# Performance work log

Measured on AMD Instinct MI355X. Metric: run time of the kernel, lower is better.

## Reference

```python
import jax, jax.numpy as jnp
import numpy as np
from jax import lax

B, C, H, W = 2, 64, 128, 128
F_SCALE, STRIDE = 2, 2
F = F_SCALE * STRIDE            # pixel-unshuffle factor = 4
CK = C // 16                    # attention channel dim = 4
SCALE_DIM = C // F_SCALE        # softmax scale uses embed_size//f_scale = 32


def setup_inputs() -> dict:
    key = jax.random.key(0)
    ks = jax.random.split(key, 16)
    g = lambda i, shape, s=0.05: jax.random.normal(ks[i], shape, jnp.float32) * s
    return {
        "x":   jax.random.normal(ks[0], (B, C, H, W), jnp.float32),
        # conv1 = Sequential(1x1 C->CK, 1x1 CK->CK)
        "w1a": g(1, (CK, C)), "b1a": g(2, (CK,)),
        "w1b": g(3, (CK, CK)), "b1b": g(4, (CK,)),
        # wqk parameter (torch.randn, std 1)
        "wqk": jax.random.normal(ks[5], (CK, CK), jnp.float32),
        # conv2: 1x1 CK->C ; conv: 1x1 C->C
        "w2":  g(6, (C, CK)), "b2": g(7, (C,)),
        "wc":  g(8, (C, C)), "bc": g(9, (C,)),
        # FF (GridSANaive): 1x1 C->C/4, 3x3 dilated C/4->C/4, 1x1 C/4->C
        "wf1": g(10, (C // 4, C)), "bf1": g(11, (C // 4,)),
        "wf2": g(12, (C // 4, C // 4, 3, 3)), "bf2": g(13, (C // 4,)),
        "wf3": g(14, (C, C // 4)), "bf3": g(15, (C,)),
    }


def conv1x1(x, w, b):
    return jnp.einsum('bchw,oc->bohw', x, w) + b[None, :, None, None]


def grid_attention(x, wqk):
    b, c, h, w = x.shape
    sh = h // 2
    x = jnp.pad(x, ((0, 0), (0, 0), (sh, 0), (0, 0)))      # Shift2d pad (top)
    # F.layer_norm over last 3 dims, no affine, eps=1e-5
    mu = jnp.mean(x, axis=(1, 2, 3), keepdims=True)
    var = jnp.var(x, axis=(1, 2, 3), keepdims=True)
    xx = (x - mu) / jnp.sqrt(var + 1e-5)
    hh, ww = xx.shape[2], xx.shape[3]
    ph, pw = (F - hh % F) % F, (F - ww % F) % F
    xx = jnp.pad(xx, ((0, 0), (0, 0), (0, ph), (0, pw)))
    gh, gw = (hh + ph) // F, (ww + pw) // F
    # pixel_unshuffle: channel layout (c, fy, fx)
    xx = xx.reshape(b, c, gh, F, gw, F).transpose(0, 1, 3, 5, 2, 4)
    xx = xx.reshape(b, c * F * F, gh, gw)
    # rearrange 'b (f c) h w -> (b f) c h w', f=F*F (mixes layout, as in original)
    xx = xx.reshape(b * F * F, c, gh, gw)
    L = gh * gw
    tok = xx.transpose(0, 2, 3, 1).reshape(b * F * F, L, c)   # (bg, L, c)
    qk = tok @ wqk
    qk = qk / (jnp.linalg.norm(qk, axis=-1, keepdims=True) + 1e-8)
    attn = (jnp.einsum('blk,bmk->blm', qk, qk) + 1.0) / (SCALE_DIM ** 0.5)
    attn = jax.nn.softmax(attn, axis=-1)
    out = jnp.einsum('blm,bmc->blc', attn, tok)
    out = out.reshape(b * F * F, gh, gw, c).transpose(0, 3, 1, 2)
    out = out.reshape(b, F * F * c, gh, gw)
    # pixel_shuffle: channel layout (fy, fx, c)
    out = out.reshape(b, F, F, c, gh, gw).transpose(0, 3, 4, 1, 5, 2)
    out = out.reshape(b, c, gh * F, gw * F)
    out = out[:, :, :hh, :ww]                               # undo shuffle pad
    return out[:, :, :-sh, :] if sh > 0 else out            # Shift2d crop (bottom)


def ff(x, wf1, bf1, wf2, bf2, wf3, bf3):
    h1 = jax.nn.relu(conv1x1(x, wf1, bf1))
    k = 1 + (STRIDE // 2) * 2   # ShiftConv2d offset for 3x3, dilation=STRIDE
    hp = jnp.pad(h1, ((0, 0), (0, 0), (k, 0), (0, 0)))
    h2 = lax.conv_general_dilated(
        hp, wf2, (1, 1), ((STRIDE, STRIDE), (STRIDE, STRIDE)),
        rhs_dilation=(STRIDE, STRIDE),
        dimension_numbers=('NCHW', 'OIHW', 'NCHW'))
    h2 = jax.nn.relu((h2 + bf2[None, :, None, None])[:, :, :-k, :])
    return conv1x1(h2, wf3, bf3)


def reference(x, w1a, b1a, w1b, b1b, wqk, w2, b2, wc, bc,
              wf1, bf1, wf2, bf2, wf3, bf3):
    a = conv1x1(conv1x1(x, w1a, b1a), w1b, b1b)
    att = grid_attention(a, wqk)
    y = x + conv1x1(conv1x1(att, w2, b2), wc, bc)
    return y + ff(y, wf1, bf1, wf2, bf2, wf3, bf3)
```

## Files before the change

kernel.cpp:

```cpp
#include <hip/hip_runtime.h>
#include <math.h>

#define CHW  (64*16384)
#define ATT_SCALE 0.17677669529663687f

__device__ __forceinline__ float poly_exp(float d) {
  return 1.f + d*(1.f + d*(0.5f + d*(0.16666667f + d*0.04166667f)));
}

__global__ __launch_bounds__(256) void k1_a_stats(
    const float* __restrict__ x, const float* __restrict__ w1a,
    const float* __restrict__ b1a, const float* __restrict__ w1b,
    const float* __restrict__ b1b, float* __restrict__ a,
    float* __restrict__ statsbuf) {
  __shared__ float sA[256];
  __shared__ float sb1[4];
  __shared__ float pc[4][4][256];
  __shared__ float rs[64], rq[64];
  int tid = threadIdx.x;
  {
    int o = tid >> 6, c = tid & 63;
    float s = 0.f;
    #pragma unroll
    for (int k = 0; k < 4; ++k) s += w1b[o*4+k] * w1a[k*64+c];
    sA[tid] = s;
  }
  if (tid < 4) {
    float s = b1b[tid];
    #pragma unroll
    for (int k = 0; k < 4; ++k) s += w1b[tid*4+k] * b1a[k];
    sb1[tid] = s;
  }
  __syncthreads();
  int quad = tid & 15, cg = tid >> 4;
  int gq = blockIdx.x * 16 + quad;
  int bb = gq >> 12;
  int px0 = (gq & 4095) * 4;
  const float* xp = x + bb*CHW + (cg*4)*16384 + px0;
  float4 acc[4];
  #pragma unroll
  for (int o = 0; o < 4; ++o) acc[o] = make_float4(0.f,0.f,0.f,0.f);
  #pragma unroll
  for (int cc = 0; cc < 4; ++cc) {
    float4 xv = *(const float4*)(xp + cc*16384);
    int c = cg*4 + cc;
    #pragma unroll
    for (int o = 0; o < 4; ++o) {
      float w = sA[o*64+c];
      acc[o].x += w*xv.x; acc[o].y += w*xv.y; acc[o].z += w*xv.z; acc[o].w += w*xv.w;
    }
  }
  #pragma unroll
  for (int o = 0; o < 4; ++o) {
    pc[0][o][tid] = acc[o].x; pc[1][o][tid] = acc[o].y;
    pc[2][o][tid] = acc[o].z; pc[3][o][tid] = acc[o].w;
  }
  __syncthreads();
  if (tid < 64) {
    int q2 = tid & 15, o = tid >> 4;
    float sx=0.f, sy=0.f, sz=0.f, sw=0.f;
    #pragma unroll
    for (int g2 = 0; g2 < 16; ++g2) {
      int idx = g2*16 + q2;
      sx += pc[0][o][idx]; sy += pc[1][o][idx];
      sz += pc[2][o][idx]; sw += pc[3][o][idx];
    }
    float bv = sb1[o];
    sx += bv; sy += bv; sz += bv; sw += bv;
    int gq2 = blockIdx.x*16 + q2;
    int b2 = gq2 >> 12; int p0 = (gq2 & 4095)*4;
    *(float4*)(a + b2*4*16384 + o*16384 + p0) = make_float4(sx,sy,sz,sw);
    rs[tid] = sx+sy+sz+sw;
    rq[tid] = sx*sx+sy*sy+sz*sz+sw*sw;
  }
  __syncthreads();
  for (int s2 = 32; s2; s2 >>= 1) {
    if (tid < s2) { rs[tid] += rs[tid+s2]; rq[tid] += rq[tid+s2]; }
    __syncthreads();
  }
  if (tid == 0) { statsbuf[blockIdx.x*2] = rs[0]; statsbuf[blockIdx.x*2+1] = rq[0]; }
}

__global__ __launch_bounds__(512) void k23_attn(
    const float* __restrict__ a, const float* __restrict__ statsbuf,
    const float* __restrict__ wqk, float* __restrict__ att) {
  __shared__ float4 kq[1024];
  __shared__ float4 kt[1024];
  __shared__ float red[8][5][64];
  __shared__ float padr[8][5];
  __shared__ float swqk[16];
  __shared__ float padout[4];
  __shared__ float smu[2];
  int tid = threadIdx.x;
  if (tid < 64) {
    float s1 = 0.f, s2 = 0.f;
    #pragma unroll
    for (int r = 0; r < 8; ++r) {
      s1 += statsbuf[2*(tid*8+r)];
      s2 += statsbuf[2*(tid*8+r)+1];
    }
    #pragma unroll
    for (int m = 1; m < 64; m <<= 1) {
      s1 += __shfl_xor(s1, m);
      s2 += __shfl_xor(s2, m);
    }
    if (tid == 0) { smu[0] = s1; smu[1] = s2; }
  }
  if (tid < 16) swqk[tid] = wqk[tid];
  __syncthreads();
  float mu  = smu[0] * (1.f/98304.f);
  float var = smu[1] * (1.f/98304.f) - mu*mu;
  float rsig = rsqrtf(var + 1e-5f);
  int g = blockIdx.x >> 3, qb = blockIdx.x & 7;
  int b = g >> 4, u = (g >> 2) & 3, v = g & 3;
  const float* abase = a + ((b*4+u) << 14);
  for (int km = tid; km < 1024; km += 512) {
    int tt = 512 + km;
    int i = tt >> 5, j = tt & 31;
    int row = (i - 16)*4 + v;
    float4 tv = *(const float4*)(abase + row*128 + (j << 2));
    tv.x = (tv.x-mu)*rsig; tv.y = (tv.y-mu)*rsig;
    tv.z = (tv.z-mu)*rsig; tv.w = (tv.w-mu)*rsig;
    float q0 = tv.x*swqk[0] + tv.y*swqk[4] + tv.z*swqk[8]  + tv.w*swqk[12];
    float q1 = tv.x*swqk[1] + tv.y*swqk[5] + tv.z*swqk[9]  + tv.w*swqk[13];
    float q2 = tv.x*swqk[2] + tv.y*swqk[6] + tv.z*swqk[10] + tv.w*swqk[14];
    float q3 = tv.x*swqk[3] + tv.y*swqk[7] + tv.z*swqk[11] + tv.w*swqk[15];
    float nrm = sqrtf(q0*q0 + q1*q1 + q2*q2 + q3*q3);
    float inv = 1.f / (nrm + 1e-8f);
    kt[km] = tv;
    kq[km] = make_float4(q0*inv, q1*inv, q2*inv, q3*inv);
  }
  float tpad = -mu * rsig;
  float c0 = swqk[0]+swqk[4]+swqk[8]+swqk[12];
  float c1 = swqk[1]+swqk[5]+swqk[9]+swqk[13];
  float c2 = swqk[2]+swqk[6]+swqk[10]+swqk[14];
  float c3 = swqk[3]+swqk[7]+swqk[11]+swqk[15];
  float p0 = tpad*c0, p1 = tpad*c1, p2 = tpad*c2, p3 = tpad*c3;
  float pn = sqrtf(p0*p0+p1*p1+p2*p2+p3*p3);
  float pinv = 1.f / (pn + 1e-8f);
  float4 qpu = make_float4(p0*pinv, p1*pinv, p2*pinv, p3*pinv);
  __syncthreads();
  int s = tid >> 5, qi = tid & 31;
  float4 q[2];
  #pragma unroll
  for (int j = 0; j < 2; ++j) {
    float4 vq = kq[qb*64 + j*32 + qi];
    q[j] = make_float4(vq.x*ATT_SCALE, vq.y*ATT_SCALE, vq.z*ATT_SCALE, vq.w*ATT_SCALE);
  }
  float den[2] = {0.f, 0.f};
  float4 ov[2];
  ov[0] = make_float4(0.f,0.f,0.f,0.f); ov[1] = make_float4(0.f,0.f,0.f,0.f);
  if (s == 0) {
    #pragma unroll
    for (int j = 0; j < 2; ++j) {
      float d = q[j].x*qpu.x + q[j].y*qpu.y + q[j].z*qpu.z + q[j].w*qpu.w;
      float e = 512.f * poly_exp(d);
      den[j] += e;
      ov[j].x += e*tpad; ov[j].y += e*tpad; ov[j].z += e*tpad; ov[j].w += e*tpad;
    }
  }
  int m0 = s * 64;
  #pragma unroll 2
  for (int m = m0; m < m0 + 64; ++m) {
    float4 kk = kq[m];
    float4 tv = kt[m];
    #pragma unroll
    for (int j = 0; j < 2; ++j) {
      float d = q[j].x*kk.x + q[j].y*kk.y + q[j].z*kk.z + q[j].w*kk.w;
      float e = poly_exp(d);
      den[j] += e;
      ov[j].x += e*tv.x; ov[j].y += e*tv.y; ov[j].z += e*tv.z; ov[j].w += e*tv.w;
    }
  }
  #pragma unroll
  for (int j = 0; j < 2; ++j) {
    den[j]  += __shfl_xor(den[j], 32);
    ov[j].x += __shfl_xor(ov[j].x, 32);
    ov[j].y += __shfl_xor(ov[j].y, 32);
    ov[j].z += __shfl_xor(ov[j].z, 32);
    ov[j].w += __shfl_xor(ov[j].w, 32);
  }
  if ((tid & 32) == 0) {
    int hs = s >> 1;
    #pragma unroll
    for (int j = 0; j < 2; ++j) {
      int slot = j*32 + qi;
      red[hs][0][slot] = den[j];
      red[hs][1][slot] = ov[j].x; red[hs][2][slot] = ov[j].y;
      red[hs][3][slot] = ov[j].z; red[hs][4][slot] = ov[j].w;
    }
  }
  {
    float4 qs = make_float4(qpu.x*ATT_SCALE, qpu.y*ATT_SCALE, qpu.z*ATT_SCALE, qpu.w*ATT_SCALE);
    float pd = 0.f, px = 0.f, py = 0.f, pz = 0.f, pw = 0.f;
    #pragma unroll
    for (int mm = 0; mm < 2; ++mm) {
      int m = tid + mm*512;
      float4 kk = kq[m]; float4 tv = kt[m];
      float d = qs.x*kk.x + qs.y*kk.y + qs.z*kk.z + qs.w*kk.w;
      float e = poly_exp(d);
      pd += e; px += e*tv.x; py += e*tv.y; pz += e*tv.z; pw += e*tv.w;
    }
    if (tid == 0) {
      float d = qs.x*qpu.x + qs.y*qpu.y + qs.z*qpu.z + qs.w*qpu.w;
      float e = 512.f * poly_exp(d);
      pd += e; px += e*tpad; py += e*tpad; pz += e*tpad; pw += e*tpad;
    }
    #pragma unroll
    for (int mask = 1; mask < 64; mask <<= 1) {
      pd += __shfl_xor(pd, mask);
      px += __shfl_xor(px, mask); py += __shfl_xor(py, mask);
      pz += __shfl_xor(pz, mask); pw += __shfl_xor(pw, mask);
    }
    if ((tid & 63) == 0) {
      int wv = tid >> 6;
      padr[wv][0] = pd; padr[wv][1] = px; padr[wv][2] = py;
      padr[wv][3] = pz; padr[wv][4] = pw;
    }
  }
  __syncthreads();
  if (tid < 64) {
    float dsum=0.f, ox=0.f, oy=0.f, oz=0.f, ow=0.f;
    #pragma unroll
    for (int ss = 0; ss < 8; ++ss) {
      dsum += red[ss][0][tid];
      ox += red[ss][1][tid]; oy += red[ss][2][tid];
      oz += red[ss][3][tid]; ow += red[ss][4][tid];
    }
    float inv = 1.f / dsum;
    int t = 512 + qb*64 + tid;
    int i = t >> 5, j = t & 31;
    float* ap = att + b*65536 + (i*4+u)*128 + (j*4+v);
    ap[0]     = ox*inv;
    ap[16384] = oy*inv;
    ap[32768] = oz*inv;
    ap[49152] = ow*inv;
  } else if (tid == 64) {
    float dsum=0.f, ox=0.f, oy=0.f, oz=0.f, ow=0.f;
    #pragma unroll
    for (int wv = 0; wv < 8; ++wv) {
      dsum += padr[wv][0];
      ox += padr[wv][1]; oy += padr[wv][2]; oz += padr[wv][3]; ow += padr[wv][4];
    }
    float inv = 1.f / dsum;
    padout[0] = ox*inv; padout[1] = oy*inv; padout[2] = oz*inv; padout[3] = ow*inv;
  }
  __syncthreads();
  if (qb == 0) {
    int i = tid >> 5, j = tid & 31;
    float* ap = att + b*65536 + (i*4+u)*128 + (j*4+v);
    ap[0] = padout[0]; ap[16384] = padout[1];
    ap[32768] = padout[2]; ap[49152] = padout[3];
  }
}

__global__ __launch_bounds__(256) void k4_y_h1(
    const float* __restrict__ x, const float* __restrict__ att,
    const float* __restrict__ w2p, const float* __restrict__ b2p,
    const float* __restrict__ wcp, const float* __restrict__ bcp,
    const float* __restrict__ wf1, const float* __restrict__ bf1,
    float* __restrict__ yout, float* __restrict__ h1) {
  __shared__ float4 sWf4[64];
  __shared__ float sbfc[64];
  __shared__ float sw1t[1024];
  __shared__ float sb1[16];
  __shared__ float4 satt[4][8];
  __shared__ float4 ylds[64][8];
  int tid = threadIdx.x;
  {
    int o = tid >> 2, k = tid & 3;
    float s = 0.f;
    for (int c = 0; c < 64; ++c) s += wcp[o*64+c] * w2p[c*4+k];
    ((float*)&sWf4[o])[k] = s;
  }
  if (tid < 64) {
    float s = bcp[tid];
    for (int c = 0; c < 64; ++c) s += wcp[tid*64+c] * b2p[c];
    sbfc[tid] = s;
  }
  for (int i = tid; i < 1024; i += 256) {
    int c = i >> 4, o2 = i & 15;
    sw1t[i] = wf1[o2*64 + c];
  }
  if (tid < 16) sb1[tid] = bf1[tid];
  int quad = tid & 7, og = tid >> 3;
  int gq = blockIdx.x*8 + quad;
  int bb = gq >> 12, px0 = (gq & 4095)*4;
  if (tid < 32) {
    int k = tid >> 3, q2 = tid & 7;
    int gq2 = blockIdx.x*8 + q2;
    int b2i = gq2 >> 12, p0 = (gq2 & 4095)*4;
    satt[k][q2] = *(const float4*)(att + b2i*65536 + k*16384 + p0);
  }
  __syncthreads();
  float4 a0 = satt[0][quad], a1 = satt[1][quad], a2 = satt[2][quad], a3 = satt[3][quad];
  const float* xp = x + bb*CHW + px0;
  float* yp = yout + bb*CHW + px0;
  #pragma unroll
  for (int cc = 0; cc < 2; ++cc) {
    int c = og*2 + cc;
    float4 xv = *(const float4*)(xp + c*16384);
    float4 wf = sWf4[c];
    float bv = sbfc[c];
    float4 yv;
    yv.x = xv.x + wf.x*a0.x + wf.y*a1.x + wf.z*a2.x + wf.w*a3.x + bv;
    yv.y = xv.y + wf.x*a0.y + wf.y*a1.y + wf.z*a2.y + wf.w*a3.y + bv;
    yv.z = xv.z + wf.x*a0.z + wf.y*a1.z + wf.z*a2.z + wf.w*a3.z + bv;
    yv.w = xv.w + wf.x*a0.w + wf.y*a1.w + wf.z*a2.w + wf.w*a3.w + bv;
    *(float4*)(yp + c*16384) = yv;
    ylds[c][quad] = yv;
  }
  __syncthreads();
  if (og < 16) {
    float bv = sb1[og];
    float4 acc = make_float4(bv, bv, bv, bv);
    #pragma unroll 8
    for (int c = 0; c < 64; ++c) {
      float w = sw1t[c*16 + og];
      float4 yv = ylds[c][quad];
      acc.x += w*yv.x; acc.y += w*yv.y; acc.z += w*yv.z; acc.w += w*yv.w;
    }
    acc.x = fmaxf(acc.x,0.f); acc.y = fmaxf(acc.y,0.f);
    acc.z = fmaxf(acc.z,0.f); acc.w = fmaxf(acc.w,0.f);
    *(float4*)(h1 + bb*262144 + og*16384 + px0) = acc;
  }
}

__global__ __launch_bounds__(256) void k6_ff_out(
    const float* __restrict__ h1, const float* __restrict__ wf2,
    const float* __restrict__ bf2, const float* __restrict__ wf3,
    const float* __restrict__ bf3, float* yo) {
  __shared__ float sbuf[16][3][40];
  __shared__ float sW2t[2304];
  __shared__ float sw3[1024];
  __shared__ float sb2[16], sb3[64];
  __shared__ float sh2[32][17];
  int tid = threadIdx.x;
  int bi = blockIdx.x;
  int bb = bi >> 9, h = (bi >> 2) & 127, wq = bi & 3;
  int W0 = wq * 32;
  for (int idx = tid; idx < 1920; idx += 256) {
    int c = idx / 120;
    int rem = idx % 120;
    int r = rem / 40, cl = rem % 40;
    int row = h - 5 + 2*r;
    int gw = W0 - 4 + cl;
    float v = 0.f;
    if (row >= 0 && gw >= 0 && gw < 128)
      v = h1[bb*262144 + c*16384 + row*128 + gw];
    sbuf[c][r][cl] = v;
  }
  for (int i2 = tid; i2 < 2304; i2 += 256) {
    int o2 = i2 & 15, rest = i2 >> 4;
    int t = rest % 3, r = (rest/3) % 3, c = rest/9;
    sW2t[i2] = wf2[((o2*16 + c)*3 + r)*3 + t];
  }
  for (int i2 = tid; i2 < 1024; i2 += 256) sw3[i2] = wf3[i2];
  if (tid < 16) sb2[tid] = bf2[tid];
  else if (tid < 80) sb3[tid-16] = bf3[tid-16];
  __syncthreads();
  int w = tid & 31, og = tid >> 5;
  float acc0 = sb2[og*2], acc1 = sb2[og*2+1];
  #pragma unroll 4
  for (int c = 0; c < 16; ++c) {
    #pragma unroll
    for (int r = 0; r < 3; ++r) {
      float tm = sbuf[c][r][w+2];
      float t0 = sbuf[c][r][w+4];
      float tp = sbuf[c][r][w+6];
      int base = ((c*3 + r)*3) << 4;
      acc0 += sW2t[base + og*2]      * tm + sW2t[base + 16 + og*2]     * t0 + sW2t[base + 32 + og*2]     * tp;
      acc1 += sW2t[base + og*2 + 1]  * tm + sW2t[base + 16 + og*2 + 1] * t0 + sW2t[base + 32 + og*2 + 1] * tp;
    }
  }
  sh2[w][og*2]   = fmaxf(acc0, 0.f);
  sh2[w][og*2+1] = fmaxf(acc1, 0.f);
  __syncthreads();
  float hv[16];
  #pragma unroll
  for (int k = 0; k < 16; ++k) hv[k] = sh2[w][k];
  float* ybase = yo + bb*CHW + h*128 + W0 + w;
  #pragma unroll 2
  for (int oc = 0; oc < 8; ++oc) {
    int o = og*8 + oc;
    float sv = sb3[o] + ybase[o*16384];
    const float* s3 = &sw3[o*16];
    #pragma unroll
    for (int k = 0; k < 16; ++k) sv += s3[k]*hv[k];
    ybase[o*16384] = sv;
  }
}

extern "C" void kernel_launch(void* const* d_in, const int* in_sizes, int n_in,
                              void* d_out, int out_size, void* d_ws, size_t ws_size,
                              hipStream_t stream) {
  (void)in_sizes; (void)n_in; (void)out_size; (void)ws_size;
  const float* x   = (const float*)d_in[0];
  const float* w1a = (const float*)d_in[1];
  const float* b1a = (const float*)d_in[2];
  const float* w1b = (const float*)d_in[3];
  const float* b1b = (const float*)d_in[4];
  const float* wqk = (const float*)d_in[5];
  const float* w2  = (const float*)d_in[6];
  const float* b2  = (const float*)d_in[7];
  const float* wc  = (const float*)d_in[8];
  const float* bc  = (const float*)d_in[9];
  const float* wf1 = (const float*)d_in[10];
  const float* bf1 = (const float*)d_in[11];
  const float* wf2 = (const float*)d_in[12];
  const float* bf2 = (const float*)d_in[13];
  const float* wf3 = (const float*)d_in[14];
  const float* bf3 = (const float*)d_in[15];

  float* ws = (float*)d_ws;
  float* a_    = ws;
  float* stats = ws + 131072;
  float* att   = ws + 132096;
  float* h1    = ws + 263168;
  float* y     = (float*)d_out;

  k1_a_stats<<<512,  256, 0, stream>>>(x, w1a, b1a, w1b, b1b, a_, stats);
  k23_attn  <<<256,  512, 0, stream>>>(a_, stats, wqk, att);
  k4_y_h1   <<<1024, 256, 0, stream>>>(x, att, w2, b2, wc, bc, wf1, bf1, y, h1);
  k6_ff_out <<<1024, 256, 0, stream>>>(h1, wf2, bf2, wf3, bf3, y);
}
```

Before: 138.4 us.

## Fuse four kernels into one cooperative persistent kernel with grid syncs

Replaces the four separate launches with a single cooperative kernel of 256 blocks of 512 threads that runs each stage in turn, separated by grid-wide syncs. Shared memory is one raw buffer reused by every stage, and each stage's work per block is remapped: stage 1 handles 32 quads per block, and the FF stage handles a full image row per block. The folded conv2/conv weights are computed once by block 0 and written to the workspace instead of being recomputed by every block. This removes inter-kernel launch gaps, but only 256 blocks cover the whole GPU, so the bandwidth-heavy stages may lose parallelism and occupancy.

Measured after the change: 231.1 us. 67.0% more time.

```diff
diff --git a/kernel.cpp b/kernel.cpp
--- a/kernel.cpp
+++ b/kernel.cpp
@@ -1,5 +1,8 @@
 #include <hip/hip_runtime.h>
+#include <hip/hip_cooperative_groups.h>
 #include <math.h>
+
+namespace cg = cooperative_groups;
 
 #define CHW  (64*16384)
 #define ATT_SCALE 0.17677669529663687f
@@ -8,386 +11,407 @@
   return 1.f + d*(1.f + d*(0.5f + d*(0.16666667f + d*0.04166667f)));
 }
 
-__global__ __launch_bounds__(256) void k1_a_stats(
+__global__ __launch_bounds__(512) void mega(
     const float* __restrict__ x, const float* __restrict__ w1a,
     const float* __restrict__ b1a, const float* __restrict__ w1b,
-    const float* __restrict__ b1b, float* __restrict__ a,
-    float* __restrict__ statsbuf) {
-  __shared__ float sA[256];
-  __shared__ float sb1[4];
-  __shared__ float pc[4][4][256];
-  __shared__ float rs[64], rq[64];
-  int tid = threadIdx.x;
-  {
-    int o = tid >> 6, c = tid & 63;
-    float s = 0.f;
-    #pragma unroll
-    for (int k = 0; k < 4; ++k) s += w1b[o*4+k] * w1a[k*64+c];
-    sA[tid] = s;
-  }
-  if (tid < 4) {
-    float s = b1b[tid];
-    #pragma unroll
-    for (int k = 0; k < 4; ++k) s += w1b[tid*4+k] * b1a[k];
-    sb1[tid] = s;
-  }
-  __syncthreads();
-  int quad = tid & 15, cg = tid >> 4;
-  int gq = blockIdx.x * 16 + quad;
-  int bb = gq >> 12;
-  int px0 = (gq & 4095) * 4;
-  const float* xp = x + bb*CHW + (cg*4)*16384 + px0;
-  float4 acc[4];
-  #pragma unroll
-  for (int o = 0; o < 4; ++o) acc[o] = make_float4(0.f,0.f,0.f,0.f);
-  #pragma unroll
-  for (int cc = 0; cc < 4; ++cc) {
-    float4 xv = *(const float4*)(xp + cc*16384);
-    int c = cg*4 + cc;
-    #pragma unroll
-    for (int o = 0; o < 4; ++o) {
-      float w = sA[o*64+c];
-      acc[o].x += w*xv.x; acc[o].y += w*xv.y; acc[o].z += w*xv.z; acc[o].w += w*xv.w;
-    }
-  }
-  #pragma unroll
-  for (int o = 0; o < 4; ++o) {
-    pc[0][o][tid] = acc[o].x; pc[1][o][tid] = acc[o].y;
-    pc[2][o][tid] = acc[o].z; pc[3][o][tid] = acc[o].w;
-  }
-  __syncthreads();
-  if (tid < 64) {
-    int q2 = tid & 15, o = tid >> 4;
-    float sx=0.f, sy=0.f, sz=0.f, sw=0.f;
-    #pragma unroll
-    for (int g2 = 0; g2 < 16; ++g2) {
-      int idx = g2*16 + q2;
-      sx += pc[0][o][idx]; sy += pc[1][o][idx];
-      sz += pc[2][o][idx]; sw += pc[3][o][idx];
-    }
-    float bv = sb1[o];
-    sx += bv; sy += bv; sz += bv; sw += bv;
-    int gq2 = blockIdx.x*16 + q2;
-    int b2 = gq2 >> 12; int p0 = (gq2 & 4095)*4;
-    *(float4*)(a + b2*4*16384 + o*16384 + p0) = make_float4(sx,sy,sz,sw);
-    rs[tid] = sx+sy+sz+sw;
-    rq[tid] = sx*sx+sy*sy+sz*sz+sw*sw;
-  }
-  __syncthreads();
-  for (int s2 = 32; s2; s2 >>= 1) {
-    if (tid < s2) { rs[tid] += rs[tid+s2]; rq[tid] += rq[tid+s2]; }
-    __syncthreads();
-  }
-  if (tid == 0) { statsbuf[blockIdx.x*2] = rs[0]; statsbuf[blockIdx.x*2+1] = rq[0]; }
-}
-
-__global__ __launch_bounds__(512) void k23_attn(
-    const float* __restrict__ a, const float* __restrict__ statsbuf,
-    const float* __restrict__ wqk, float* __restrict__ att) {
-  __shared__ float4 kq[1024];
-  __shared__ float4 kt[1024];
-  __shared__ float red[8][5][64];
-  __shared__ float padr[8][5];
-  __shared__ float swqk[16];
-  __shared__ float padout[4];
-  __shared__ float smu[2];
-  int tid = threadIdx.x;
-  if (tid < 64) {
-    float s1 = 0.f, s2 = 0.f;
-    #pragma unroll
-    for (int r = 0; r < 8; ++r) {
-      s1 += statsbuf[2*(tid*8+r)];
-      s2 += statsbuf[2*(tid*8+r)+1];
-    }
-    #pragma unroll
-    for (int m = 1; m < 64; m <<= 1) {
-      s1 += __shfl_xor(s1, m);
-      s2 += __shfl_xor(s2, m);
-    }
-    if (tid == 0) { smu[0] = s1; smu[1] = s2; }
-  }
-  if (tid < 16) swqk[tid] = wqk[tid];
-  __syncthreads();
-  float mu  = smu[0] * (1.f/98304.f);
-  float var = smu[1] * (1.f/98304.f) - mu*mu;
-  float rsig = rsqrtf(var + 1e-5f);
-  int g = blockIdx.x >> 3, qb = blockIdx.x & 7;
-  int b = g >> 4, u = (g >> 2) & 3, v = g & 3;
-  const float* abase = a + ((b*4+u) << 14);
-  for (int km = tid; km < 1024; km += 512) {
-    int tt = 512 + km;
-    int i = tt >> 5, j = tt & 31;
-    int row = (i - 16)*4 + v;
-    float4 tv = *(const float4*)(abase + row*128 + (j << 2));
-    tv.x = (tv.x-mu)*rsig; tv.y = (tv.y-mu)*rsig;
-    tv.z = (tv.z-mu)*rsig; tv.w = (tv.w-mu)*rsig;
-    float q0 = tv.x*swqk[0] + tv.y*swqk[4] + tv.z*swqk[8]  + tv.w*swqk[12];
-    float q1 = tv.x*swqk[1] + tv.y*swqk[5] + tv.z*swqk[9]  + tv.w*swqk[13];
-    float q2 = tv.x*swqk[2] + tv.y*swqk[6] + tv.z*swqk[10] + tv.w*swqk[14];
-    float q3 = tv.x*swqk[3] + tv.y*swqk[7] + tv.z*swqk[11] + tv.w*swqk[15];
-    float nrm = sqrtf(q0*q0 + q1*q1 + q2*q2 + q3*q3);
-    float inv = 1.f / (nrm + 1e-8f);
-    kt[km] = tv;
-    kq[km] = make_float4(q0*inv, q1*inv, q2*inv, q3*inv);
-  }
-  float tpad = -mu * rsig;
-  float c0 = swqk[0]+swqk[4]+swqk[8]+swqk[12];
-  float c1 = swqk[1]+swqk[5]+swqk[9]+swqk[13];
-  float c2 = swqk[2]+swqk[6]+swqk[10]+swqk[14];
-  float c3 = swqk[3]+swqk[7]+swqk[11]+swqk[15];
-  float p0 = tpad*c0, p1 = tpad*c1, p2 = tpad*c2, p3 = tpad*c3;
-  float pn = sqrtf(p0*p0+p1*p1+p2*p2+p3*p3);
-  float pinv = 1.f / (pn + 1e-8f);
-  float4 qpu = make_float4(p0*pinv, p1*pinv, p2*pinv, p3*pinv);
-  __syncthreads();
-  int s = tid >> 5, qi = tid & 31;
-  float4 q[2];
-  #pragma unroll
-  for (int j = 0; j < 2; ++j) {
-    float4 vq = kq[qb*64 + j*32 + qi];
-    q[j] = make_float4(vq.x*ATT_SCALE, vq.y*ATT_SCALE, vq.z*ATT_SCALE, vq.w*ATT_SCALE);
-  }
-  float den[2] = {0.f, 0.f};
-  float4 ov[2];
-  ov[0] = make_float4(0.f,0.f,0.f,0.f); ov[1] = make_float4(0.f,0.f,0.f,0.f);
-  if (s == 0) {
-    #pragma unroll
-    for (int j = 0; j < 2; ++j) {
-      float d = q[j].x*qpu.x + q[j].y*qpu.y + q[j].z*qpu.z + q[j].w*qpu.w;
-      float e = 512.f * poly_exp(d);
-      den[j] += e;
-      ov[j].x += e*tpad; ov[j].y += e*tpad; ov[j].z += e*tpad; ov[j].w += e*tpad;
-    }
-  }
-  int m0 = s * 64;
-  #pragma unroll 2
-  for (int m = m0; m < m0 + 64; ++m) {
-    float4 kk = kq[m];
-    float4 tv = kt[m];
-    #pragma unroll
-    for (int j = 0; j < 2; ++j) {
-      float d = q[j].x*kk.x + q[j].y*kk.y + q[j].z*kk.z + q[j].w*kk.w;
-      float e = poly_exp(d);
-      den[j] += e;
-      ov[j].x += e*tv.x; ov[j].y += e*tv.y; ov[j].z += e*tv.z; ov[j].w += e*tv.w;
-    }
-  }
-  #pragma unroll
-  for (int j = 0; j < 2; ++j) {
-    den[j]  += __shfl_xor(den[j], 32);
-    ov[j].x += __shfl_xor(ov[j].x, 32);
-    ov[j].y += __shfl_xor(ov[j].y, 32);
-    ov[j].z += __shfl_xor(ov[j].z, 32);
-    ov[j].w += __shfl_xor(ov[j].w, 32);
-  }
-  if ((tid & 32) == 0) {
-    int hs = s >> 1;
-    #pragma unroll
-    for (int j = 0; j < 2; ++j) {
-      int slot = j*32 + qi;
-      red[hs][0][slot] = den[j];
-      red[hs][1][slot] = ov[j].x; red[hs][2][slot] = ov[j].y;
-      red[hs][3][slot] = ov[j].z; red[hs][4][slot] = ov[j].w;
-    }
-  }
-  {
-    float4 qs = make_float4(qpu.x*ATT_SCALE, qpu.y*ATT_SCALE, qpu.z*ATT_SCALE, qpu.w*ATT_SCALE);
-    float pd = 0.f, px = 0.f, py = 0.f, pz = 0.f, pw = 0.f;
-    #pragma unroll
-    for (int mm = 0; mm < 2; ++mm) {
-      int m = tid + mm*512;
-      float4 kk = kq[m]; float4 tv = kt[m];
-      float d = qs.x*kk.x + qs.y*kk.y + qs.z*kk.z + qs.w*kk.w;
-      float e = poly_exp(d);
-      pd += e; px += e*tv.x; py += e*tv.y; pz += e*tv.z; pw += e*tv.w;
-    }
-    if (tid == 0) {
-      float d = qs.x*qpu.x + qs.y*qpu.y + qs.z*qpu.z + qs.w*qpu.w;
-      float e = 512.f * poly_exp(d);
-      pd += e; px += e*tpad; py += e*tpad; pz += e*tpad; pw += e*tpad;
-    }
-    #pragma unroll
-    for (int mask = 1; mask < 64; mask <<= 1) {
-      pd += __shfl_xor(pd, mask);
-      px += __shfl_xor(px, mask); py += __shfl_xor(py, mask);
-      pz += __shfl_xor(pz, mask); pw += __shfl_xor(pw, mask);
-    }
-    if ((tid & 63) == 0) {
-      int wv = tid >> 6;
-      padr[wv][0] = pd; padr[wv][1] = px; padr[wv][2] = py;
-      padr[wv][3] = pz; padr[wv][4] = pw;
-    }
-  }
-  __syncthreads();
-  if (tid < 64) {
-    float dsum=0.f, ox=0.f, oy=0.f, oz=0.f, ow=0.f;
-    #pragma unroll
-    for (int ss = 0; ss < 8; ++ss) {
-      dsum += red[ss][0][tid];
-      ox += red[ss][1][tid]; oy += red[ss][2][tid];
-      oz += red[ss][3][tid]; ow += red[ss][4][tid];
-    }
-    float inv = 1.f / dsum;
-    int t = 512 + qb*64 + tid;
-    int i = t >> 5, j = t & 31;
-    float* ap = att + b*65536 + (i*4+u)*128 + (j*4+v);
-    ap[0]     = ox*inv;
-    ap[16384] = oy*inv;
-    ap[32768] = oz*inv;
-    ap[49152] = ow*inv;
-  } else if (tid == 64) {
-    float dsum=0.f, ox=0.f, oy=0.f, oz=0.f, ow=0.f;
-    #pragma unroll
-    for (int wv = 0; wv < 8; ++wv) {
-      dsum += padr[wv][0];
-      ox += padr[wv][1]; oy += padr[wv][2]; oz += padr[wv][3]; ow += padr[wv][4];
-    }
-    float inv = 1.f / dsum;
-    padout[0] = ox*inv; padout[1] = oy*inv; padout[2] = oz*inv; padout[3] = ow*inv;
-  }
-  __syncthreads();
-  if (qb == 0) {
-    int i = tid >> 5, j = tid & 31;
-    float* ap = att + b*65536 + (i*4+u)*128 + (j*4+v);
-    ap[0] = padout[0]; ap[16384] = padout[1];
-    ap[32768] = padout[2]; ap[49152] = padout[3];
-  }
-}
-
-__global__ __launch_bounds__(256) void k4_y_h1(
-    const float* __restrict__ x, const float* __restrict__ att,
+    const float* __restrict__ b1b, const float* __restrict__ wqk,
     const float* __restrict__ w2p, const float* __restrict__ b2p,
     const float* __restrict__ wcp, const float* __restrict__ bcp,
     const float* __restrict__ wf1, const float* __restrict__ bf1,
-    float* __restrict__ yout, float* __restrict__ h1) {
-  __shared__ float4 sWf4[64];
-  __shared__ float sbfc[64];
-  __shared__ float sw1t[1024];
-  __shared__ float sb1[16];
-  __shared__ float4 satt[4][8];
-  __shared__ float4 ylds[64][8];
+    const float* __restrict__ wf2, const float* __restrict__ bf2,
+    const float* __restrict__ wf3, const float* __restrict__ bf3,
+    float* __restrict__ a, float* __restrict__ statsbuf,
+    float* __restrict__ att, float* __restrict__ h1,
+    float* __restrict__ wfold, float* out) {
+  __shared__ __align__(16) char smraw[48448];
+  cg::grid_group gg = cg::this_grid();
   int tid = threadIdx.x;
+  int bi = blockIdx.x;
+
   {
-    int o = tid >> 2, k = tid & 3;
-    float s = 0.f;
-    for (int c = 0; c < 64; ++c) s += wcp[o*64+c] * w2p[c*4+k];
-    ((float*)&sWf4[o])[k] = s;
+    float* sA  = (float*)smraw;
+    float* pc  = (float*)(smraw + 1024);
+    float* rs  = (float*)(smraw + 33792);
+    float* rq  = (float*)(smraw + 34304);
+    float* sb1 = (float*)(smraw + 34816);
+    if (tid < 256) {
+      int o = tid >> 6, c = tid & 63;
+      float s = 0.f;
+      #pragma unroll
+      for (int k = 0; k < 4; ++k) s += w1b[o*4+k] * w1a[k*64+c];
+      sA[tid] = s;
+    }
+    if (tid < 4) {
+      float s = b1b[tid];
+      #pragma unroll
+      for (int k = 0; k < 4; ++k) s += w1b[tid*4+k] * b1a[k];
+      sb1[tid] = s;
+    }
+    __syncthreads();
+    int quad = tid & 31, cgi = tid >> 5;
+    int gq = bi*32 + quad;
+    int bb = gq >> 12, px0 = (gq & 4095) * 4;
+    const float* xp = x + bb*CHW + (cgi*4)*16384 + px0;
+    float4 acc[4];
+    #pragma unroll
+    for (int o = 0; o < 4; ++o) acc[o] = make_float4(0.f,0.f,0.f,0.f);
+    #pragma unroll
+    for (int cc = 0; cc < 4; ++cc) {
+      float4 xv = *(const float4*)(xp + cc*16384);
+      int c = cgi*4 + cc;
+      #pragma unroll
+      for (int o = 0; o < 4; ++o) {
+        float w = sA[o*64+c];
+        acc[o].x += w*xv.x; acc[o].y += w*xv.y; acc[o].z += w*xv.z; acc[o].w += w*xv.w;
+      }
+    }
+    #pragma unroll
+    for (int o = 0; o < 4; ++o) {
+      pc[((0*4+o)<<9) + tid] = acc[o].x;
+      pc[((1*4+o)<<9) + tid] = acc[o].y;
+      pc[((2*4+o)<<9) + tid] = acc[o].z;
+      pc[((3*4+o)<<9) + tid] = acc[o].w;
+    }
+    __syncthreads();
+    if (tid < 128) {
+      int q2 = tid & 31, o = tid >> 5;
+      float sx=0.f, sy=0.f, sz=0.f, sw=0.f;
+      #pragma unroll
+      for (int g2 = 0; g2 < 16; ++g2) {
+        int idx = g2*32 + q2;
+        sx += pc[((0*4+o)<<9) + idx];
+        sy += pc[((1*4+o)<<9) + idx];
+        sz += pc[((2*4+o)<<9) + idx];
+        sw += pc[((3*4+o)<<9) + idx];
+      }
+      float bv = sb1[o];
+      sx += bv; sy += bv; sz += bv; sw += bv;
+      int gq2 = bi*32 + q2;
+      int b2 = gq2 >> 12, p0 = (gq2 & 4095)*4;
+      *(float4*)(a + b2*65536 + o*16384 + p0) = make_float4(sx,sy,sz,sw);
+      rs[tid] = sx+sy+sz+sw;
+      rq[tid] = sx*sx+sy*sy+sz*sz+sw*sw;
+    }
+    __syncthreads();
+    if (tid < 64) {
+      float s1 = rs[tid] + rs[tid+64];
+      float s2 = rq[tid] + rq[tid+64];
+      #pragma unroll
+      for (int m = 1; m < 64; m <<= 1) {
+        s1 += __shfl_xor(s1, m);
+        s2 += __shfl_xor(s2, m);
+      }
+      if (tid == 0) { statsbuf[bi*2] = s1; statsbuf[bi*2+1] = s2; }
+    }
+    if (bi == 0) {
+      if (tid < 256) {
+        int o = tid >> 2, k = tid & 3;
+        float s = 0.f;
+        for (int c = 0; c < 64; ++c) s += wcp[o*64+c] * w2p[c*4+k];
+        wfold[tid] = s;
+      } else if (tid < 320) {
+        int o = tid - 256;
+        float s = bcp[o];
+        for (int c = 0; c < 64; ++c) s += wcp[o*64+c] * b2p[c];
+        wfold[256+o] = s;
+      }
+    }
   }
-  if (tid < 64) {
-    float s = bcp[tid];
-    for (int c = 0; c < 64; ++c) s += wcp[tid*64+c] * b2p[c];
-    sbfc[tid] = s;
+  gg.sync();
+
+  {
+    float4* kq = (float4*)smraw;
+    float4* kt = (float4*)(smraw + 16384);
+    float*  red = (float*)(smraw + 32768);
+    float*  padr = (float*)(smraw + 43008);
+    float*  swqk = (float*)(smraw + 43168);
+    float*  padout = (float*)(smraw + 43232);
+    float*  smu = (float*)(smraw + 43248);
+    if (tid < 64) {
+      float s1 = 0.f, s2 = 0.f;
+      #pragma unroll
+      for (int r = 0; r < 4; ++r) {
+        s1 += statsbuf[2*(tid*4+r)];
+        s2 += statsbuf[2*(tid*4+r)+1];
+      }
+      #pragma unroll
+      for (int m = 1; m < 64; m <<= 1) {
+        s1 += __shfl_xor(s1, m);
+        s2 += __shfl_xor(s2, m);
+      }
+      if (tid == 0) { smu[0] = s1; smu[1] = s2; }
+    }
+    if (tid < 16) swqk[tid] = wqk[tid];
+    __syncthreads();
+    float mu  = smu[0] * (1.f/98304.f);
+    float var = smu[1] * (1.f/98304.f) - mu*mu;
+    float rsig = rsqrtf(var + 1e-5f);
+    int g = bi >> 3, qb = bi & 7;
+    int b = g >> 4, u = (g >> 2) & 3, v = g & 3;
+    const float* abase = a + ((b*4+u) << 14);
+    for (int km = tid; km < 1024; km += 512) {
+      int tt = 512 + km;
+      int i = tt >> 5, j = tt & 31;
+      int row = (i - 16)*4 + v;
+      float4 tv = *(const float4*)(abase + row*128 + (j << 2));
+      tv.x = (tv.x-mu)*rsig; tv.y = (tv.y-mu)*rsig;
+      tv.z = (tv.z-mu)*rsig; tv.w = (tv.w-mu)*rsig;
+      float q0 = tv.x*swqk[0] + tv.y*swqk[4] + tv.z*swqk[8]  + tv.w*swqk[12];
+      float q1 = tv.x*swqk[1] + tv.y*swqk[5] + tv.z*swqk[9]  + tv.w*swqk[13];
+      float q2 = tv.x*swqk[2] + tv.y*swqk[6] + tv.z*swqk[10] + tv.w*swqk[14];
+      float q3 = tv.x*swqk[3] + tv.y*swqk[7] + tv.z*swqk[11] + tv.w*swqk[15];
+      float nrm = sqrtf(q0*q0 + q1*q1 + q2*q2 + q3*q3);
+      float inv = 1.f / (nrm + 1e-8f);
+      kt[km] = tv;
+      kq[km] = make_float4(q0*inv, q1*inv, q2*inv, q3*inv);
+    }
+    float tpad = -mu * rsig;
+    float c0 = swqk[0]+swqk[4]+swqk[8]+swqk[12];
+    float c1 = swqk[1]+swqk[5]+swqk[9]+swqk[13];
+    float c2 = swqk[2]+swqk[6]+swqk[10]+swqk[14];
+    float c3 = swqk[3]+swqk[7]+swqk[11]+swqk[15];
+    float p0 = tpad*c0, p1 = tpad*c1, p2 = tpad*c2, p3 = tpad*c3;
+    float pn = sqrtf(p0*p0+p1*p1+p2*p2+p3*p3);
+    float pinv = 1.f / (pn + 1e-8f);
+    float4 qpu = make_float4(p0*pinv, p1*pinv, p2*pinv, p3*pinv);
+    __syncthreads();
+    int s = tid >> 5, qi = tid & 31;
+    float4 q[2];
+    #pragma unroll
+    for (int j = 0; j < 2; ++j) {
+      float4 vq = kq[qb*64 + j*32 + qi];
+      q[j] = make_float4(vq.x*ATT_SCALE, vq.y*ATT_SCALE, vq.z*ATT_SCALE, vq.w*ATT_SCALE);
+    }
+    float den[2] = {0.f, 0.f};
+    float4 ov[2];
+    ov[0] = make_float4(0.f,0.f,0.f,0.f); ov[1] = make_float4(0.f,0.f,0.f,0.f);
+    if (s == 0) {
+      #pragma unroll
+      for (int j = 0; j < 2; ++j) {
+        float d = q[j].x*qpu.x + q[j].y*qpu.y + q[j].z*qpu.z + q[j].w*qpu.w;
+        float e = 512.f * poly_exp(d);
+        den[j] += e;
+        ov[j].x += e*tpad; ov[j].y += e*tpad; ov[j].z += e*tpad; ov[j].w += e*tpad;
+      }
+    }
+    int m0 = s * 64;
+    #pragma unroll 2
+    for (int m = m0; m < m0 + 64; ++m) {
+      float4 kk = kq[m];
+      float4 tv = kt[m];
+      #pragma unroll
+      for (int j = 0; j < 2; ++j) {
+        float d = q[j].x*kk.x + q[j].y*kk.y + q[j].z*kk.z + q[j].w*kk.w;
+        float e = poly_exp(d);
+        den[j] += e;
+        ov[j].x += e*tv.x; ov[j].y += e*tv.y; ov[j].z += e*tv.z; ov[j].w += e*tv.w;
+      }
+    }
+    #pragma unroll
+    for (int j = 0; j < 2; ++j) {
+      den[j]  += __shfl_xor(den[j], 32);
+      ov[j].x += __shfl_xor(ov[j].x, 32);
+      ov[j].y += __shfl_xor(ov[j].y, 32);
+      ov[j].z += __shfl_xor(ov[j].z, 32);
+      ov[j].w += __shfl_xor(ov[j].w, 32);
+    }
+    if ((tid & 32) == 0) {
+      int hs = s >> 1;
+      #pragma unroll
+      for (int j = 0; j < 2; ++j) {
+        int slot = j*32 + qi;
+        red[(hs*5+0)*64+slot] = den[j];
+        red[(hs*5+1)*64+slot] = ov[j].x; red[(hs*5+2)*64+slot] = ov[j].y;
+        red[(hs*5+3)*64+slot] = ov[j].z; red[(hs*5+4)*64+slot] = ov[j].w;
+      }
+    }
+    {
+      float4 qs = make_float4(qpu.x*ATT_SCALE, qpu.y*ATT_SCALE, qpu.z*ATT_SCALE, qpu.w*ATT_SCALE);
+      float pd = 0.f, px = 0.f, py = 0.f, pz = 0.f, pw = 0.f;
+      #pragma unroll
+      for (int mm = 0; mm < 2; ++mm) {
+        int m = tid + mm*512;
+        float4 kk = kq[m]; float4 tv = kt[m];
+        float d = qs.x*kk.x + qs.y*kk.y + qs.z*kk.z + qs.w*kk.w;
+        float e = poly_exp(d);
+        pd += e; px += e*tv.x; py += e*tv.y; pz += e*tv.z; pw += e*tv.w;
+      }
+      if (tid == 0) {
+        float d = qs.x*qpu.x + qs.y*qpu.y + qs.z*qpu.z + qs.w*qpu.w;
+        float e = 512.f * poly_exp(d);
+        pd += e; px += e*tpad; py += e*tpad; pz += e*tpad; pw += e*tpad;
+      }
+      #pragma unroll
+      for (int mask = 1; mask < 64; mask <<= 1) {
+        pd += __shfl_xor(pd, mask);
+        px += __shfl_xor(px, mask); py += __shfl_xor(py, mask);
+        pz += __shfl_xor(pz, mask); pw += __shfl_xor(pw, mask);
+      }
+      if ((tid & 63) == 0) {
+        int wv = tid >> 6;
+        padr[wv*5+0] = pd; padr[wv*5+1] = px; padr[wv*5+2] = py;
+        padr[wv*5+3] = pz; padr[wv*5+4] = pw;
+      }
+    }
+    __syncthreads();
+    if (tid < 64) {
+      float dsum=0.f, ox=0.f, oy=0.f, oz=0.f, ow=0.f;
+      #pragma unroll
+      for (int ss = 0; ss < 8; ++ss) {
+        dsum += red[(ss*5+0)*64+tid];
+        ox += red[(ss*5+1)*64+tid]; oy += red[(ss*5+2)*64+tid];
+        oz += red[(ss*5+3)*64+tid]; ow += red[(ss*5+4)*64+tid];
+      }
+      float inv = 1.f / dsum;
+      int t = 512 + qb*64 + tid;
+      int i = t >> 5, j = t & 31;
+      float* ap = att + b*65536 + (i*4+u)*128 + (j*4+v);
+      ap[0]     = ox*inv;
+      ap[16384] = oy*inv;
+      ap[32768] = oz*inv;
+      ap[49152] = ow*inv;
+    } else if (tid == 64) {
+      float dsum=0.f, ox=0.f, oy=0.f, oz=0.f, ow=0.f;
+      #pragma unroll
+      for (int wv = 0; wv < 8; ++wv) {
+        dsum += padr[wv*5+0];
+        ox += padr[wv*5+1]; oy += padr[wv*5+2]; oz += padr[wv*5+3]; ow += padr[wv*5+4];
+      }
+      float inv = 1.f / dsum;
+      padout[0] = ox*inv; padout[1] = oy*inv; padout[2] = oz*inv; padout[3] = ow*inv;
+    }
+    __syncthreads();
+    if (qb == 0) {
+      int i = tid >> 5, j = tid & 31;
+      float* ap = att + b*65536 + (i*4+u)*128 + (j*4+v);
+      ap[0] = padout[0]; ap[16384] = padout[1];
+      ap[32768] = padout[2]; ap[49152] = padout[3];
+    }
   }
-  for (int i = tid; i < 1024; i += 256) {
-    int c = i >> 4, o2 = i & 15;
-    sw1t[i] = wf1[o2*64 + c];
-  }
-  if (tid < 16) sb1[tid] = bf1[tid];
-  int quad = tid & 7, og = tid >> 3;
-  int gq = blockIdx.x*8 + quad;
-  int bb = gq >> 12, px0 = (gq & 4095)*4;
-  if (tid < 32) {
-    int k = tid >> 3, q2 = tid & 7;
-    int gq2 = blockIdx.x*8 + q2;
-    int b2i = gq2 >> 12, p0 = (gq2 & 4095)*4;
-    satt[k][q2] = *(const float4*)(att + b2i*65536 + k*16384 + p0);
-  }
-  __syncthreads();
-  float4 a0 = satt[0][quad], a1 = satt[1][quad], a2 = satt[2][quad], a3 = satt[3][quad];
-  const float* xp = x + bb*CHW + px0;
-  float* yp = yout + bb*CHW + px0;
-  #pragma unroll
-  for (int cc = 0; cc < 2; ++cc) {
-    int c = og*2 + cc;
-    float4 xv = *(const float4*)(xp + c*16384);
-    float4 wf = sWf4[c];
-    float bv = sbfc[c];
-    float4 yv;
-    yv.x = xv.x + wf.x*a0.x + wf.y*a1.x + wf.z*a2.x + wf.w*a3.x + bv;
-    yv.y = xv.y + wf.x*a0.y + wf.y*a1.y + wf.z*a2.y + wf.w*a3.y + bv;
-    yv.z = xv.z + wf.x*a0.z + wf.y*a1.z + wf.z*a2.z + wf.w*a3.z + bv;
-    yv.w = xv.w + wf.x*a0.w + wf.y*a1.w + wf.z*a2.w + wf.w*a3.w + bv;
-    *(float4*)(yp + c*16384) = yv;
-    ylds[c][quad] = yv;
-  }
-  __syncthreads();
-  if (og < 16) {
+  gg.sync();
+
+  {
+    float4* sWf4 = (float4*)smraw;
+    float*  sbfc = (float*)(smraw + 1024);
+    float*  sw1t = (float*)(smraw + 1280);
+    float*  sb1  = (float*)(smraw + 5376);
+    float4* satt = (float4*)(smraw + 5440);
+    float4* ylds = (float4*)(smraw + 7488);
+    if (tid < 64) sWf4[tid] = ((const float4*)wfold)[tid];
+    else if (tid < 128) sbfc[tid-64] = wfold[256 + tid - 64];
+    for (int i = tid; i < 1024; i += 512) sw1t[i] = wf1[(i & 15)*64 + (i >> 4)];
+    if (tid < 16) sb1[tid] = bf1[tid];
+    int quad = tid & 31, og = tid >> 5;
+    int gq = bi*32 + quad;
+    int bb = gq >> 12, px0 = (gq & 4095)*4;
+    if (tid < 128) {
+      int k = tid >> 5, q2 = tid & 31;
+      int gq2 = bi*32 + q2;
+      int b2i = gq2 >> 12, p0 = (gq2 & 4095)*4;
+      satt[k*32+q2] = *(const float4*)(att + b2i*65536 + k*16384 + p0);
+    }
+    __syncthreads();
+    float4 a0 = satt[0*32+quad], a1 = satt[1*32+quad],
+           a2 = satt[2*32+quad], a3 = satt[3*32+quad];
+    const float* xp = x + bb*CHW + px0;
+    float* yp = out + bb*CHW + px0;
+    #pragma unroll
+    for (int cc = 0; cc < 4; ++cc) {
+      int c = og*4 + cc;
+      float4 xv = *(const float4*)(xp + c*16384);
+      float4 wf = sWf4[c];
+      float bv = sbfc[c];
+      float4 yv;
+      yv.x = xv.x + wf.x*a0.x + wf.y*a1.x + wf.z*a2.x + wf.w*a3.x + bv;
+      yv.y = xv.y + wf.x*a0.y + wf.y*a1.y + wf.z*a2.y + wf.w*a3.y + bv;
+      yv.z = xv.z + wf.x*a0.z + wf.y*a1.z + wf.z*a2.z + wf.w*a3.z + bv;
+      yv.w = xv.w + wf.x*a0.w + wf.y*a1.w + wf.z*a2.w + wf.w*a3.w + bv;
+      *(float4*)(yp + c*16384) = yv;
+      ylds[c*32+quad] = yv;
+    }
+    __syncthreads();
     float bv = sb1[og];
     float4 acc = make_float4(bv, bv, bv, bv);
     #pragma unroll 8
     for (int c = 0; c < 64; ++c) {
       float w = sw1t[c*16 + og];
-      float4 yv = ylds[c][quad];
+      float4 yv = ylds[c*32+quad];
       acc.x += w*yv.x; acc.y += w*yv.y; acc.z += w*yv.z; acc.w += w*yv.w;
     }
     acc.x = fmaxf(acc.x,0.f); acc.y = fmaxf(acc.y,0.f);
     acc.z = fmaxf(acc.z,0.f); acc.w = fmaxf(acc.w,0.f);
     *(float4*)(h1 + bb*262144 + og*16384 + px0) = acc;
   }
-}
-
-__global__ __launch_bounds__(256) void k6_ff_out(
-    const float* __restrict__ h1, const float* __restrict__ wf2,
-    const float* __restrict__ bf2, const float* __restrict__ wf3,
-    const float* __restrict__ bf3, float* yo) {
-  __shared__ float sbuf[16][3][40];
-  __shared__ float sW2t[2304];
-  __shared__ float sw3[1024];
-  __shared__ float sb2[16], sb3[64];
-  __shared__ float sh2[32][17];
-  int tid = threadIdx.x;
-  int bi = blockIdx.x;
-  int bb = bi >> 9, h = (bi >> 2) & 127, wq = bi & 3;
-  int W0 = wq * 32;
-  for (int idx = tid; idx < 1920; idx += 256) {
-    int c = idx / 120;
-    int rem = idx % 120;
-    int r = rem / 40, cl = rem % 40;
-    int row = h - 5 + 2*r;
-    int gw = W0 - 4 + cl;
-    float v = 0.f;
-    if (row >= 0 && gw >= 0 && gw < 128)
-      v = h1[bb*262144 + c*16384 + row*128 + gw];
-    sbuf[c][r][cl] = v;
-  }
-  for (int i2 = tid; i2 < 2304; i2 += 256) {
-    int o2 = i2 & 15, rest = i2 >> 4;
-    int t = rest % 3, r = (rest/3) % 3, c = rest/9;
-    sW2t[i2] = wf2[((o2*16 + c)*3 + r)*3 + t];
-  }
-  for (int i2 = tid; i2 < 1024; i2 += 256) sw3[i2] = wf3[i2];
-  if (tid < 16) sb2[tid] = bf2[tid];
-  else if (tid < 80) sb3[tid-16] = bf3[tid-16];
-  __syncthreads();
-  int w = tid & 31, og = tid >> 5;
-  float acc0 = sb2[og*2], acc1 = sb2[og*2+1];
-  #pragma unroll 4
-  for (int c = 0; c < 16; ++c) {
-    #pragma unroll
-    for (int r = 0; r < 3; ++r) {
-      float tm = sbuf[c][r][w+2];
-      float t0 = sbuf[c][r][w+4];
-      float tp = sbuf[c][r][w+6];
-      int base = ((c*3 + r)*3) << 4;
-      acc0 += sW2t[base + og*2]      * tm + sW2t[base + 16 + og*2]     * t0 + sW2t[base + 32 + og*2]     * tp;
-      acc1 += sW2t[base + og*2 + 1]  * tm + sW2t[base + 16 + og*2 + 1] * t0 + sW2t[base + 32 + og*2 + 1] * tp;
-    }
-  }
-  sh2[w][og*2]   = fmaxf(acc0, 0.f);
-  sh2[w][og*2+1] = fmaxf(acc1, 0.f);
-  __syncthreads();
-  float hv[16];
-  #pragma unroll
-  for (int k = 0; k < 16; ++k) hv[k] = sh2[w][k];
-  float* ybase = yo + bb*CHW + h*128 + W0 + w;
-  #pragma unroll 2
-  for (int oc = 0; oc < 8; ++oc) {
-    int o = og*8 + oc;
-    float sv = sb3[o] + ybase[o*16384];
-    const float* s3 = &sw3[o*16];
-    #pragma unroll
-    for (int k = 0; k < 16; ++k) sv += s3[k]*hv[k];
-    ybase[o*16384] = sv;
+  gg.sync();
+
+  {
+    float* sbuf = (float*)smraw;
+    float* sW2t = (float*)(smraw + 26112);
+    float* sw3  = (float*)(smraw + 35328);
+    float* sb2  = (float*)(smraw + 39424);
+    float* sb3  = (float*)(smraw + 39488);
+    float* sh2  = (float*)(smraw + 39744);
+    int bb = bi >> 7, h = bi & 127;
+    for (int idx = tid; idx < 6528; idx += 512) {
+      int c = idx / 408;
+      int rem = idx - c*408;
+      int r = rem / 136, cl = rem - r*136;
+      int row = h - 5 + 2*r;
+      int gw = cl - 4;
+      float v = 0.f;
+      if (row >= 0 && gw >= 0 && gw < 128)
+        v = h1[bb*262144 + c*16384 + row*128 + gw];
+      sbuf[(c*3+r)*136 + cl] = v;
+    }
+    for (int i2 = tid; i2 < 2304; i2 += 512) {
+      int o2 = i2 & 15, rest = i2 >> 4;
+      int t = rest % 3, r = (rest/3) % 3, c = rest/9;
+      sW2t[i2] = wf2[((o2*16 + c)*3 + r)*3 + t];
+    }
+    for (int i2 = tid; i2 < 1024; i2 += 512) sw3[i2] = wf3[i2];
+    if (tid < 16) sb2[tid] = bf2[tid];
+    else if (tid < 80) sb3[tid-16] = bf3[tid-16];
+    __syncthreads();
+    int w = tid & 127, og = tid >> 7;
+    float h2[4];
+    #pragma unroll
+    for (int o = 0; o < 4; ++o) h2[o] = sb2[og*4+o];
+    for (int c = 0; c < 16; ++c) {
+      #pragma unroll
+      for (int r = 0; r < 3; ++r) {
+        const float* sb = &sbuf[(c*3+r)*136];
+        float tm = sb[w+2];
+        float t0 = sb[w+4];
+        float tp = sb[w+6];
+        int base = ((c*3 + r)*3) << 4;
+        float4 w0 = *(const float4*)&sW2t[base + og*4];
+        float4 w1 = *(const float4*)&sW2t[base + 16 + og*4];
+        float4 w2v = *(const float4*)&sW2t[base + 32 + og*4];
+        h2[0] += w0.x*tm + w1.x*t0 + w2v.x*tp;
+        h2[1] += w0.y*tm + w1.y*t0 + w2v.y*tp;
+        h2[2] += w0.z*tm + w1.z*t0 + w2v.z*tp;
+        h2[3] += w0.w*tm + w1.w*t0 + w2v.w*tp;
+      }
+    }
+    #pragma unroll
+    for (int o = 0; o < 4; ++o) sh2[w*17 + og*4+o] = fmaxf(h2[o], 0.f);
+    __syncthreads();
+    float hv[16];
+    #pragma unroll
+    for (int k = 0; k < 16; ++k) hv[k] = sh2[w*17 + k];
+    float* ybase = out + bb*CHW + h*128 + w;
+    #pragma unroll 4
+    for (int oc = 0; oc < 16; ++oc) {
+      int o = og*16 + oc;
+      float sv = sb3[o] + ybase[o*16384];
+      const float4* s3 = (const float4*)&sw3[o*16];
+      float4 s30 = s3[0], s31 = s3[1], s32 = s3[2], s33 = s3[3];
+      sv += s30.x*hv[0] + s30.y*hv[1] + s30.z*hv[2] + s30.w*hv[3];
+      sv += s31.x*hv[4] + s31.y*hv[5] + s31.z*hv[6] + s31.w*hv[7];
+      sv += s32.x*hv[8] + s32.y*hv[9] + s32.z*hv[10] + s32.w*hv[11];
+      sv += s33.x*hv[12] + s33.y*hv[13] + s33.z*hv[14] + s33.w*hv[15];
+      ybase[o*16384] = sv;
+    }
   }
 }
 
@@ -417,10 +441,14 @@
   float* stats = ws + 131072;
   float* att   = ws + 132096;
   float* h1    = ws + 263168;
-  float* y     = (float*)d_out;
-
-  k1_a_stats<<<512,  256, 0, stream>>>(x, w1a, b1a, w1b, b1b, a_, stats);
-  k23_attn  <<<256,  512, 0, stream>>>(a_, stats, wqk, att);
-  k4_y_h1   <<<1024, 256, 0, stream>>>(x, att, w2, b2, wc, bc, wf1, bf1, y, h1);
-  k6_ff_out <<<1024, 256, 0, stream>>>(h1, wf2, bf2, wf3, bf3, y);
+  float* wfold = ws + 787456;
+  float* out   = (float*)d_out;
+
+  void* args[] = {
+    (void*)&x, (void*)&w1a, (void*)&b1a, (void*)&w1b, (void*)&b1b, (void*)&wqk,
+    (void*)&w2, (void*)&b2, (void*)&wc, (void*)&bc,
+    (void*)&wf1, (void*)&bf1, (void*)&wf2, (void*)&bf2, (void*)&wf3, (void*)&bf3,
+    (void*)&a_, (void*)&stats, (void*)&att, (void*)&h1, (void*)&wfold, (void*)&out
+  };
+  hipLaunchCooperativeKernel((const void*)mega, dim3(256), dim3(512), args, 0, stream);
 }
```

## Precompute folded output weights once and trim redundant attention and reduction work

Applied to the files above, without the earlier changes.

The folded wc·w2 weight matrix and bias are now computed once by block 0 of the first kernel and stored in the workspace. Each block of the y/h1 kernel loads them instead of recomputing a 64x64 reduction per block. The padding-token attention pass is restricted to qb==0 blocks, the only ones that consume its result. The stats tree reduction in the first kernel is replaced with a wavefront shuffle reduction. This relies on the kernel ordering on the stream so the folded weights are written before the y/h1 kernel reads them.

Result: no change. 135.9 us (-1.8%).

```diff
diff --git a/kernel.cpp b/kernel.cpp
--- a/kernel.cpp
+++ b/kernel.cpp
@@ -11,8 +11,11 @@
 __global__ __launch_bounds__(256) void k1_a_stats(
     const float* __restrict__ x, const float* __restrict__ w1a,
     const float* __restrict__ b1a, const float* __restrict__ w1b,
-    const float* __restrict__ b1b, float* __restrict__ a,
-    float* __restrict__ statsbuf) {
+    const float* __restrict__ b1b,
+    const float* __restrict__ w2p, const float* __restrict__ b2p,
+    const float* __restrict__ wcp, const float* __restrict__ bcp,
+    float* __restrict__ a, float* __restrict__ statsbuf,
+    float* __restrict__ wfold) {
   __shared__ float sA[256];
   __shared__ float sb1[4];
   __shared__ float pc[4][4][256];
@@ -31,6 +34,19 @@
     for (int k = 0; k < 4; ++k) s += w1b[tid*4+k] * b1a[k];
     sb1[tid] = s;
   }
+  if (blockIdx.x == 0) {
+    {
+      int o = tid >> 2, k = tid & 3;
+      float s = 0.f;
+      for (int c = 0; c < 64; ++c) s += wcp[o*64+c] * w2p[c*4+k];
+      wfold[tid] = s;
+    }
+    if (tid < 64) {
+      float s = bcp[tid];
+      for (int c = 0; c < 64; ++c) s += wcp[tid*64+c] * b2p[c];
+      wfold[256+tid] = s;
+    }
+  }
   __syncthreads();
   int quad = tid & 15, cg = tid >> 4;
   int gq = blockIdx.x * 16 + quad;
@@ -74,11 +90,15 @@
     rq[tid] = sx*sx+sy*sy+sz*sz+sw*sw;
   }
   __syncthreads();
-  for (int s2 = 32; s2; s2 >>= 1) {
-    if (tid < s2) { rs[tid] += rs[tid+s2]; rq[tid] += rq[tid+s2]; }
-    __syncthreads();
-  }
-  if (tid == 0) { statsbuf[blockIdx.x*2] = rs[0]; statsbuf[blockIdx.x*2+1] = rq[0]; }
+  if (tid < 64) {
+    float s1 = rs[tid], s2 = rq[tid];
+    #pragma unroll
+    for (int m = 1; m < 64; m <<= 1) {
+      s1 += __shfl_xor(s1, m);
+      s2 += __shfl_xor(s2, m);
+    }
+    if (tid == 0) { statsbuf[blockIdx.x*2] = s1; statsbuf[blockIdx.x*2+1] = s2; }
+  }
 }
 
 __global__ __launch_bounds__(512) void k23_attn(
@@ -190,7 +210,7 @@
       red[hs][3][slot] = ov[j].z; red[hs][4][slot] = ov[j].w;
     }
   }
-  {
+  if (qb == 0) {
     float4 qs = make_float4(qpu.x*ATT_SCALE, qpu.y*ATT_SCALE, qpu.z*ATT_SCALE, qpu.w*ATT_SCALE);
     float pd = 0.f, px = 0.f, py = 0.f, pz = 0.f, pw = 0.f;
     #pragma unroll
@@ -235,7 +255,7 @@
     ap[16384] = oy*inv;
     ap[32768] = oz*inv;
     ap[49152] = ow*inv;
-  } else if (tid == 64) {
+  } else if (qb == 0 && tid == 64) {
     float dsum=0.f, ox=0.f, oy=0.f, oz=0.f, ow=0.f;
     #pragma unroll
     for (int wv = 0; wv < 8; ++wv) {
@@ -256,8 +276,7 @@
 
 __global__ __launch_bounds__(256) void k4_y_h1(
     const float* __restrict__ x, const float* __restrict__ att,
-    const float* __restrict__ w2p, const float* __restrict__ b2p,
-    const float* __restrict__ wcp, const float* __restrict__ bcp,
+    const float* __restrict__ wfold,
     const float* __restrict__ wf1, const float* __restrict__ bf1,
     float* __restrict__ yout, float* __restrict__ h1) {
   __shared__ float4 sWf4[64];
@@ -267,17 +286,8 @@
   __shared__ float4 satt[4][8];
   __shared__ float4 ylds[64][8];
   int tid = threadIdx.x;
-  {
-    int o = tid >> 2, k = tid & 3;
-    float s = 0.f;
-    for (int c = 0; c < 64; ++c) s += wcp[o*64+c] * w2p[c*4+k];
-    ((float*)&sWf4[o])[k] = s;
-  }
-  if (tid < 64) {
-    float s = bcp[tid];
-    for (int c = 0; c < 64; ++c) s += wcp[tid*64+c] * b2p[c];
-    sbfc[tid] = s;
-  }
+  if (tid < 64) sWf4[tid] = ((const float4*)wfold)[tid];
+  else if (tid < 128) sbfc[tid-64] = wfold[256 + tid - 64];
   for (int i = tid; i < 1024; i += 256) {
     int c = i >> 4, o2 = i & 15;
     sw1t[i] = wf1[o2*64 + c];
@@ -417,10 +427,12 @@
   float* stats = ws + 131072;
   float* att   = ws + 132096;
   float* h1    = ws + 263168;
+  float* wfold = ws + 787456;
   float* y     = (float*)d_out;
 
-  k1_a_stats<<<512,  256, 0, stream>>>(x, w1a, b1a, w1b, b1b, a_, stats);
+  k1_a_stats<<<512,  256, 0, stream>>>(x, w1a, b1a, w1b, b1b, w2, b2, wc, bc,
+                                       a_, stats, wfold);
   k23_attn  <<<256,  512, 0, stream>>>(a_, stats, wqk, att);
-  k4_y_h1   <<<1024, 256, 0, stream>>>(x, att, w2, b2, wc, bc, wf1, bf1, y, h1);
+  k4_y_h1   <<<1024, 256, 0, stream>>>(x, att, wfold, wf1, bf1, y, h1);
   k6_ff_out <<<1024, 256, 0, stream>>>(h1, wf2, bf2, wf3, bf3, y);
 }
```
